# Optimization experiments

Hardware: AMD Instinct MI355X
Metric: run time of the kernel (lower is better)

The kernel has to match this reference:

```python
import jax, jax.numpy as jnp
import numpy as np

N_NODES = 50000


def _gcn_norm(edge_index, num_nodes):
    # PyG GCNConv default: add self-loops, symmetric normalization D^-1/2 A D^-1/2
    src, dst = edge_index[0], edge_index[1]
    loops = jnp.arange(num_nodes, dtype=src.dtype)
    src = jnp.concatenate([src, loops])
    dst = jnp.concatenate([dst, loops])
    deg = jax.ops.segment_sum(jnp.ones_like(src, dtype=jnp.float32), dst,
                              num_segments=num_nodes)
    dis = jnp.where(deg > 0, jax.lax.rsqrt(jnp.maximum(deg, 1.0)), 0.0)
    norm = dis[src] * dis[dst]  # [E']
    return src, dst, norm


def _gcn_conv(x, W, b, src, dst, norm, num_nodes):
    h = x @ W                                   # [N, out] transform first
    msg = h[src] * norm[:, None]                # [E', out] gather + scale
    agg = jax.ops.segment_sum(msg, dst, num_segments=num_nodes)  # scatter-add
    return agg + b


def setup_inputs() -> dict:
    key = jax.random.key(0)
    k1, k2, k3, k4 = jax.random.split(key, 4)
    n, e, d_in, d_h = N_NODES, 800000, 256, 128
    basic_block = jax.random.normal(k1, (n, d_in), dtype=jnp.float32)
    edge_index = jax.random.randint(k2, (2, e), 0, n, dtype=jnp.int64)
    W1 = jax.random.normal(k3, (d_in, d_h), dtype=jnp.float32) * (1.0 / np.sqrt(d_in))
    b1 = jnp.zeros((d_h,), dtype=jnp.float32)
    W2 = jax.random.normal(k4, (d_h, d_h), dtype=jnp.float32) * (1.0 / np.sqrt(d_h))
    b2 = jnp.zeros((d_h,), dtype=jnp.float32)
    return {"basic_block": basic_block, "edge_index": edge_index,
            "W1": W1, "b1": b1, "W2": W2, "b2": b2}


def reference(basic_block, edge_index, W1, b1, W2, b2):
    n = basic_block.shape[0]
    src, dst, norm = _gcn_norm(edge_index, n)
    x = jax.nn.relu(_gcn_conv(basic_block, W1, b1, src, dst, norm, n))
    x = _gcn_conv(x, W2, b2, src, dst, norm, n)
    return x
```

## Files before the change

kernel.cpp:

```cpp
#include <hip/hip_runtime.h>
#include <hip/hip_bf16.h>
#include <stdint.h>

#define D_H 128

typedef __bf16 bf16_t;
typedef unsigned short u16;
typedef bf16_t bf16x8 __attribute__((ext_vector_type(8)));
typedef bf16_t bf16x4 __attribute__((ext_vector_type(4)));
typedef float  f32x4  __attribute__((ext_vector_type(4)));

__global__ void k_countrank(const int* __restrict__ dst, int* __restrict__ cnt,
                            u16* __restrict__ rank, int E, int crBlocks,
                            const float* __restrict__ W1, bf16_t* __restrict__ W1h,
                            bf16_t* __restrict__ W1l, int K1,
                            const float* __restrict__ W2, bf16_t* __restrict__ W2h,
                            bf16_t* __restrict__ W2l, int K2) {
    if ((int)blockIdx.x < crBlocks) {
        int e = blockIdx.x * 256 + threadIdx.x;
        if (e < E) rank[e] = (u16)atomicAdd(&cnt[dst[e]], 1);
        return;
    }
    int id = ((int)blockIdx.x - crBlocks) * 256 + threadIdx.x;
    int n1 = K1 * 128;
    if (id < n1) {
        int k = id >> 7, n = id & 127;
        float w = W1[id];
        bf16_t h = (bf16_t)w;
        W1h[(size_t)n * K1 + k] = h;
        W1l[(size_t)n * K1 + k] = (bf16_t)(w - (float)h);
    } else if (id < n1 + K2 * 128) {
        int id2 = id - n1;
        int k = id2 >> 7, n = id2 & 127;
        float w = W2[id2];
        bf16_t h = (bf16_t)w;
        W2h[(size_t)n * K2 + k] = h;
        W2l[(size_t)n * K2 + k] = (bf16_t)(w - (float)h);
    }
}

__global__ __launch_bounds__(1024) void k_scan1(const int* __restrict__ cnt,
                                                int* __restrict__ out,
                                                int* __restrict__ bsums,
                                                float* __restrict__ dis, int N) {
    __shared__ int tmp[1024];
    int t = threadIdx.x;
    int i = blockIdx.x * 1024 + t;
    int v = (i < N) ? cnt[i] : 0;
    if (i < N) dis[i] = 1.0f / sqrtf((float)(v + 1));
    tmp[t] = v;
    __syncthreads();
    for (int d = 1; d < 1024; d <<= 1) {
        int x = (t >= d) ? tmp[t - d] : 0;
        __syncthreads();
        tmp[t] += x;
        __syncthreads();
    }
    if (i < N) out[i] = tmp[t] - v;
    if (t == 1023) bsums[blockIdx.x] = tmp[t];
}

__global__ void k_scan2(int* __restrict__ bsums, int nb) {
    __shared__ int tmp[64];
    int t = threadIdx.x;
    int v = (t < nb) ? bsums[t] : 0;
    tmp[t] = v;
    __syncthreads();
    for (int d = 1; d < 64; d <<= 1) {
        int x = (t >= d) ? tmp[t - d] : 0;
        __syncthreads();
        tmp[t] += x;
        __syncthreads();
    }
    if (t < nb) bsums[t] = tmp[t] - v;
}

__global__ __launch_bounds__(1024) void k_scan3(int* __restrict__ off,
                                                const int* __restrict__ bsums,
                                                int N, int E) {
    int i = blockIdx.x * 1024 + threadIdx.x;
    if (i < N) off[i] += bsums[blockIdx.x];
    if (i == 0) off[N] = E;
}

#define LDK 40
#define FILL_PER 2

__global__ __launch_bounds__(256) void k_mm1fill(
        const float* __restrict__ Af,
        const bf16_t* __restrict__ Wh, const bf16_t* __restrict__ Wl,
        const float* __restrict__ dis, bf16_t* __restrict__ Cb,
        int N, int K,
        const int* __restrict__ src, const int* __restrict__ dst,
        const int* __restrict__ off, const u16* __restrict__ rank,
        u16* __restrict__ csr16, int E, int totThreads) {
    __shared__ bf16_t AsH[64][LDK];
    __shared__ bf16_t AsL[64][LDK];
    __shared__ bf16_t BsH[64][LDK];
    __shared__ bf16_t BsL[64][LDK];

    const int t    = threadIdx.x;
    const int lane = t & 63;
    const int wave = t >> 6;
    const int row0 = ((int)blockIdx.x >> 1) * 64;
    const int col0 = ((int)blockIdx.x & 1) * 64;
    const int wm   = (wave & 1) * 32;
    const int wn   = (wave >> 1) * 32;
    const int fm   = lane & 15;
    const int fq   = lane >> 4;

    const int g = (int)blockIdx.x * 256 + t;
    int epos[FILL_PER];
    u16 esrc[FILL_PER];
#pragma unroll
    for (int i = 0; i < FILL_PER; i++) {
        int e = g + i * totThreads;
        if (e < E) {
            int d = dst[e];
            epos[i] = off[d] + (int)rank[e];
            esrc[i] = (u16)src[e];
        } else {
            epos[i] = -1;
            esrc[i] = 0;
        }
    }

    f32x4 acc[2][2] = {};

    for (int k0 = 0; k0 < K; k0 += 32) {
        __syncthreads();
#pragma unroll
        for (int i = 0; i < 2; i++) {
            int idx = t + i * 256;
            int r   = idx >> 3;
            int c4  = idx & 7;
            int gr  = row0 + r;
            float4 v = make_float4(0.f, 0.f, 0.f, 0.f);
            if (gr < N) v = *(const float4*)(Af + (size_t)gr * K + k0 + c4 * 4);
            bf16_t h0 = (bf16_t)v.x, h1 = (bf16_t)v.y, h2 = (bf16_t)v.z, h3 = (bf16_t)v.w;
            bf16_t l0 = (bf16_t)(v.x - (float)h0);
            bf16_t l1 = (bf16_t)(v.y - (float)h1);
            bf16_t l2 = (bf16_t)(v.z - (float)h2);
            bf16_t l3 = (bf16_t)(v.w - (float)h3);
            *(bf16x4*)&AsH[r][c4 * 4] = (bf16x4){h0, h1, h2, h3};
            *(bf16x4*)&AsL[r][c4 * 4] = (bf16x4){l0, l1, l2, l3};
        }
        {
            int r  = t >> 2;
            int c8 = t & 3;
            *(bf16x8*)&BsH[r][c8 * 8] = *(const bf16x8*)(Wh + (size_t)(col0 + r) * K + k0 + c8 * 8);
            *(bf16x8*)&BsL[r][c8 * 8] = *(const bf16x8*)(Wl + (size_t)(col0 + r) * K + k0 + c8 * 8);
        }
        __syncthreads();

        bf16x8 ah[2], al[2], bh[2], bl[2];
#pragma unroll
        for (int i = 0; i < 2; i++) {
            ah[i] = *(const bf16x8*)&AsH[wm + i * 16 + fm][fq * 8];
            al[i] = *(const bf16x8*)&AsL[wm + i * 16 + fm][fq * 8];
            bh[i] = *(const bf16x8*)&BsH[wn + i * 16 + fm][fq * 8];
            bl[i] = *(const bf16x8*)&BsL[wn + i * 16 + fm][fq * 8];
        }
#pragma unroll
        for (int mi = 0; mi < 2; mi++)
#pragma unroll
            for (int ni = 0; ni < 2; ni++) {
                acc[mi][ni] = __builtin_amdgcn_mfma_f32_16x16x32_bf16(ah[mi], bh[ni], acc[mi][ni], 0, 0, 0);
                acc[mi][ni] = __builtin_amdgcn_mfma_f32_16x16x32_bf16(ah[mi], bl[ni], acc[mi][ni], 0, 0, 0);
                acc[mi][ni] = __builtin_amdgcn_mfma_f32_16x16x32_bf16(al[mi], bh[ni], acc[mi][ni], 0, 0, 0);
            }
    }

#pragma unroll
    for (int mi = 0; mi < 2; mi++)
#pragma unroll
        for (int r = 0; r < 4; r++) {
            int grow = row0 + wm + mi * 16 + fq * 4 + r;
            if (grow < N) {
                float dr = dis[grow];
#pragma unroll
                for (int ni = 0; ni < 2; ni++)
                    Cb[(size_t)grow * D_H + col0 + wn + ni * 16 + fm] = (bf16_t)(dr * acc[mi][ni][r]);
            }
        }

#pragma unroll
    for (int i = 0; i < FILL_PER; i++)
        if (epos[i] >= 0) csr16[epos[i]] = esrc[i];
}

__global__ __launch_bounds__(256) void k_mm2(const bf16_t* __restrict__ Ah,
                                             const bf16_t* __restrict__ Al,
                                             const bf16_t* __restrict__ Wh,
                                             const bf16_t* __restrict__ Wl,
                                             const float* __restrict__ dis,
                                             bf16_t* __restrict__ Cb,
                                             int N, int K) {
    __shared__ bf16_t AsH[64][LDK];
    __shared__ bf16_t AsL[64][LDK];
    __shared__ bf16_t BsH[64][LDK];
    __shared__ bf16_t BsL[64][LDK];

    const int t    = threadIdx.x;
    const int lane = t & 63;
    const int wave = t >> 6;
    const int row0 = ((int)blockIdx.x >> 1) * 64;
    const int col0 = ((int)blockIdx.x & 1) * 64;
    const int wm   = (wave & 1) * 32;
    const int wn   = (wave >> 1) * 32;
    const int fm   = lane & 15;
    const int fq   = lane >> 4;

    f32x4 acc[2][2] = {};

    for (int k0 = 0; k0 < K; k0 += 32) {
        __syncthreads();
        {
            int r  = t >> 2;
            int c8 = t & 3;
            int gr = row0 + r;
            bf16x8 vh = {}, vl = {};
            if (gr < N) {
                vh = *(const bf16x8*)(Ah + (size_t)gr * K + k0 + c8 * 8);
                vl = *(const bf16x8*)(Al + (size_t)gr * K + k0 + c8 * 8);
            }
            *(bf16x8*)&AsH[r][c8 * 8] = vh;
            *(bf16x8*)&AsL[r][c8 * 8] = vl;
        }
        {
            int r  = t >> 2;
            int c8 = t & 3;
            *(bf16x8*)&BsH[r][c8 * 8] = *(const bf16x8*)(Wh + (size_t)(col0 + r) * K + k0 + c8 * 8);
            *(bf16x8*)&BsL[r][c8 * 8] = *(const bf16x8*)(Wl + (size_t)(col0 + r) * K + k0 + c8 * 8);
        }
        __syncthreads();

        bf16x8 ah[2], al[2], bh[2], bl[2];
#pragma unroll
        for (int i = 0; i < 2; i++) {
            ah[i] = *(const bf16x8*)&AsH[wm + i * 16 + fm][fq * 8];
            al[i] = *(const bf16x8*)&AsL[wm + i * 16 + fm][fq * 8];
            bh[i] = *(const bf16x8*)&BsH[wn + i * 16 + fm][fq * 8];
            bl[i] = *(const bf16x8*)&BsL[wn + i * 16 + fm][fq * 8];
        }
#pragma unroll
        for (int mi = 0; mi < 2; mi++)
#pragma unroll
            for (int ni = 0; ni < 2; ni++) {
                acc[mi][ni] = __builtin_amdgcn_mfma_f32_16x16x32_bf16(ah[mi], bh[ni], acc[mi][ni], 0, 0, 0);
                acc[mi][ni] = __builtin_amdgcn_mfma_f32_16x16x32_bf16(ah[mi], bl[ni], acc[mi][ni], 0, 0, 0);
                acc[mi][ni] = __builtin_amdgcn_mfma_f32_16x16x32_bf16(al[mi], bh[ni], acc[mi][ni], 0, 0, 0);
            }
    }

#pragma unroll
    for (int mi = 0; mi < 2; mi++)
#pragma unroll
        for (int r = 0; r < 4; r++) {
            int grow = row0 + wm + mi * 16 + fq * 4 + r;
            if (grow < N) {
                float dr = dis[grow];
#pragma unroll
                for (int ni = 0; ni < 2; ni++)
                    Cb[(size_t)grow * D_H + col0 + wn + ni * 16 + fm] = (bf16_t)(dr * acc[mi][ni][r]);
            }
        }
}

__global__ __launch_bounds__(256) void k_agg(const bf16_t* __restrict__ Hb,
                                             const float* __restrict__ dis,
                                             const int* __restrict__ off,
                                             const u16* __restrict__ csr16,
                                             const float4* __restrict__ bias4,
                                             float4* __restrict__ outF,
                                             bf16_t* __restrict__ outH,
                                             bf16_t* __restrict__ outL,
                                             int N, int mode) {
    const int half = threadIdx.x >> 5;
    const int lane = threadIdx.x & 31;
    const int node = blockIdx.x * 8 + half;
    if (node >= N) return;

    const size_t loff = (size_t)lane * 4;

    bf16x4 vs = *(const bf16x4*)(Hb + (size_t)node * D_H + loff);
    float4 a0 = make_float4((float)vs[0], (float)vs[1], (float)vs[2], (float)vs[3]);
    float4 a1 = {0,0,0,0}, a2 = {0,0,0,0}, a3 = {0,0,0,0};
    float4 a4 = {0,0,0,0}, a5 = {0,0,0,0}, a6 = {0,0,0,0}, a7 = {0,0,0,0};

    int p  = off[node];
    int p1 = off[node + 1];

    for (; p + 8 <= p1; p += 8) {
        int s0 = (int)csr16[p + 0], s1 = (int)csr16[p + 1];
        int s2 = (int)csr16[p + 2], s3 = (int)csr16[p + 3];
        int s4 = (int)csr16[p + 4], s5 = (int)csr16[p + 5];
        int s6 = (int)csr16[p + 6], s7 = (int)csr16[p + 7];
        bf16x4 h0 = *(const bf16x4*)(Hb + (size_t)s0 * D_H + loff);
        bf16x4 h1 = *(const bf16x4*)(Hb + (size_t)s1 * D_H + loff);
        bf16x4 h2 = *(const bf16x4*)(Hb + (size_t)s2 * D_H + loff);
        bf16x4 h3 = *(const bf16x4*)(Hb + (size_t)s3 * D_H + loff);
        bf16x4 h4 = *(const bf16x4*)(Hb + (size_t)s4 * D_H + loff);
        bf16x4 h5 = *(const bf16x4*)(Hb + (size_t)s5 * D_H + loff);
        bf16x4 h6 = *(const bf16x4*)(Hb + (size_t)s6 * D_H + loff);
        bf16x4 h7 = *(const bf16x4*)(Hb + (size_t)s7 * D_H + loff);
        a0.x += (float)h0[0]; a0.y += (float)h0[1]; a0.z += (float)h0[2]; a0.w += (float)h0[3];
        a1.x += (float)h1[0]; a1.y += (float)h1[1]; a1.z += (float)h1[2]; a1.w += (float)h1[3];
        a2.x += (float)h2[0]; a2.y += (float)h2[1]; a2.z += (float)h2[2]; a2.w += (float)h2[3];
        a3.x += (float)h3[0]; a3.y += (float)h3[1]; a3.z += (float)h3[2]; a3.w += (float)h3[3];
        a4.x += (float)h4[0]; a4.y += (float)h4[1]; a4.z += (float)h4[2]; a4.w += (float)h4[3];
        a5.x += (float)h5[0]; a5.y += (float)h5[1]; a5.z += (float)h5[2]; a5.w += (float)h5[3];
        a6.x += (float)h6[0]; a6.y += (float)h6[1]; a6.z += (float)h6[2]; a6.w += (float)h6[3];
        a7.x += (float)h7[0]; a7.y += (float)h7[1]; a7.z += (float)h7[2]; a7.w += (float)h7[3];
    }
    if (p + 4 <= p1) {
        int s0 = (int)csr16[p + 0], s1 = (int)csr16[p + 1];
        int s2 = (int)csr16[p + 2], s3 = (int)csr16[p + 3];
        bf16x4 h0 = *(const bf16x4*)(Hb + (size_t)s0 * D_H + loff);
        bf16x4 h1 = *(const bf16x4*)(Hb + (size_t)s1 * D_H + loff);
        bf16x4 h2 = *(const bf16x4*)(Hb + (size_t)s2 * D_H + loff);
        bf16x4 h3 = *(const bf16x4*)(Hb + (size_t)s3 * D_H + loff);
        a0.x += (float)h0[0]; a0.y += (float)h0[1]; a0.z += (float)h0[2]; a0.w += (float)h0[3];
        a1.x += (float)h1[0]; a1.y += (float)h1[1]; a1.z += (float)h1[2]; a1.w += (float)h1[3];
        a2.x += (float)h2[0]; a2.y += (float)h2[1]; a2.z += (float)h2[2]; a2.w += (float)h2[3];
        a3.x += (float)h3[0]; a3.y += (float)h3[1]; a3.z += (float)h3[2]; a3.w += (float)h3[3];
        p += 4;
    }
    for (; p < p1; p++) {
        int s0 = (int)csr16[p];
        bf16x4 h0 = *(const bf16x4*)(Hb + (size_t)s0 * D_H + loff);
        a0.x += (float)h0[0]; a0.y += (float)h0[1]; a0.z += (float)h0[2]; a0.w += (float)h0[3];
    }

    float4 sum;
    sum.x = ((a0.x + a1.x) + (a2.x + a3.x)) + ((a4.x + a5.x) + (a6.x + a7.x));
    sum.y = ((a0.y + a1.y) + (a2.y + a3.y)) + ((a4.y + a5.y) + (a6.y + a7.y));
    sum.z = ((a0.z + a1.z) + (a2.z + a3.z)) + ((a4.z + a5.z) + (a6.z + a7.z));
    sum.w = ((a0.w + a1.w) + (a2.w + a3.w)) + ((a4.w + a5.w) + (a6.w + a7.w));

    const float  di = dis[node];
    const float4 bv = bias4[lane];
    float vx = fmaf(di, sum.x, bv.x);
    float vy = fmaf(di, sum.y, bv.y);
    float vz = fmaf(di, sum.z, bv.z);
    float vw = fmaf(di, sum.w, bv.w);

    if (mode == 1) {
        vx = fmaxf(vx, 0.0f); vy = fmaxf(vy, 0.0f);
        vz = fmaxf(vz, 0.0f); vw = fmaxf(vw, 0.0f);
        bf16_t hx = (bf16_t)vx, hy = (bf16_t)vy, hz = (bf16_t)vz, hw = (bf16_t)vw;
        bf16_t lx = (bf16_t)(vx - (float)hx);
        bf16_t ly = (bf16_t)(vy - (float)hy);
        bf16_t lz = (bf16_t)(vz - (float)hz);
        bf16_t lw = (bf16_t)(vw - (float)hw);
        *(bf16x4*)(outH + (size_t)node * D_H + loff) = (bf16x4){hx, hy, hz, hw};
        *(bf16x4*)(outL + (size_t)node * D_H + loff) = (bf16x4){lx, ly, lz, lw};
    } else {
        outF[(size_t)node * 32 + lane] = make_float4(vx, vy, vz, vw);
    }
}

extern "C" void kernel_launch(void* const* d_in, const int* in_sizes, int n_in,
                              void* d_out, int out_size, void* d_ws, size_t ws_size,
                              hipStream_t stream) {
    const float* X  = (const float*)d_in[0];
    const int*   ei = (const int*)d_in[1];
    const float* W1 = (const float*)d_in[2];
    const float* b1 = (const float*)d_in[3];
    const float* W2 = (const float*)d_in[4];
    const float* b2 = (const float*)d_in[5];
    float* out = (float*)d_out;

    const int N  = in_sizes[0] / 256;
    const int E  = in_sizes[1] / 2;
    const int K1 = 256;

    const int* src = ei;
    const int* dst = ei + E;

    uintptr_t p = (uintptr_t)d_ws;
    auto carve = [&](size_t bytes) {
        uintptr_t q = p;
        p += (bytes + 255) & ~(size_t)255;
        return q;
    };
    int*    cnt   = (int*)carve((size_t)N * 4);
    int*    off   = (int*)carve((size_t)(N + 1) * 4);
    int*    bsums = (int*)carve(64 * 4);
    float*  dis   = (float*)carve((size_t)N * 4);
    u16*    rank  = (u16*)carve((size_t)E * 2);
    u16*    csr16 = (u16*)carve((size_t)E * 2);
    bf16_t* Hb    = (bf16_t*)carve((size_t)N * D_H * 2);
    bf16_t* X1h   = (bf16_t*)carve((size_t)N * D_H * 2);
    bf16_t* X1l   = (bf16_t*)carve((size_t)N * D_H * 2);
    bf16_t* W1h   = (bf16_t*)carve((size_t)K1 * D_H * 2);
    bf16_t* W1l   = (bf16_t*)carve((size_t)K1 * D_H * 2);
    bf16_t* W2h   = (bf16_t*)carve((size_t)D_H * D_H * 2);
    bf16_t* W2l   = (bf16_t*)carve((size_t)D_H * D_H * 2);

    const int nb = (N + 1023) / 1024;

    hipMemsetAsync(cnt, 0, (size_t)N * 4, stream);
    const int gcr   = (E + 255) / 256;
    const int gprep = (K1 * 128 + D_H * 128 + 255) / 256;
    k_countrank<<<gcr + gprep, 256, 0, stream>>>(dst, cnt, rank, E, gcr,
                                                 W1, W1h, W1l, K1,
                                                 W2, W2h, W2l, D_H);
    k_scan1<<<nb, 1024, 0, stream>>>(cnt, off, bsums, dis, N);
    k_scan2<<<1, 64, 0, stream>>>(bsums, nb);
    k_scan3<<<nb, 1024, 0, stream>>>(off, bsums, N, E);

    const int gmm = ((N + 63) / 64) * 2;
    const int gag = (N + 7) / 8;

    k_mm1fill<<<gmm, 256, 0, stream>>>(X, W1h, W1l, dis, Hb, N, K1,
                                       src, dst, off, rank, csr16, E, gmm * 256);
    k_agg<<<gag, 256, 0, stream>>>(Hb, dis, off, csr16,
                                   (const float4*)b1, nullptr, X1h, X1l, N, 1);

    k_mm2<<<gmm, 256, 0, stream>>>(X1h, X1l, W2h, W2l, dis, Hb, N, D_H);
    k_agg<<<gag, 256, 0, stream>>>(Hb, dis, off, csr16,
                                   (const float4*)b2, (float4*)out, nullptr, nullptr, N, 0);
}
```

Before: 251.4 us.

## Replace LDS-staged GEMM tiles with direct register loads and double buffering

Both GEMM kernels no longer stage A and W tiles through shared memory with two barriers per k-step. Each lane now loads its MFMA fragments straight from global memory into registers, using two register sets so the next k-tile's loads overlap the current tile's MFMAs. This removes the LDS traffic and synchronisation, but each wave reloads data that neighbouring waves also read, which puts more load on the caches. The loops hardcode K=256 and K=128 trip counts, and out-of-range rows are clamped to N-1 rather than zero-filled.

Result: slower. 295.2 us (+17.4%).

```diff
diff --git a/kernel.cpp b/kernel.cpp
--- a/kernel.cpp
+++ b/kernel.cpp
@@ -83,7 +83,6 @@
     if (i == 0) off[N] = E;
 }
 
-#define LDK 40
 #define FILL_PER 2
 
 __global__ __launch_bounds__(256) void k_mm1fill(
@@ -94,11 +93,6 @@
         const int* __restrict__ src, const int* __restrict__ dst,
         const int* __restrict__ off, const u16* __restrict__ rank,
         u16* __restrict__ csr16, int E, int totThreads) {
-    __shared__ bf16_t AsH[64][LDK];
-    __shared__ bf16_t AsL[64][LDK];
-    __shared__ bf16_t BsH[64][LDK];
-    __shared__ bf16_t BsL[64][LDK];
-
     const int t    = threadIdx.x;
     const int lane = t & 63;
     const int wave = t >> 6;
@@ -125,51 +119,67 @@
         }
     }
 
+    int ra0 = row0 + wm + fm;      if (ra0 >= N) ra0 = N - 1;
+    int ra1 = row0 + wm + 16 + fm; if (ra1 >= N) ra1 = N - 1;
+    const float*  pa0 = Af + (size_t)ra0 * K + fq * 8;
+    const float*  pa1 = Af + (size_t)ra1 * K + fq * 8;
+    const bf16_t* pb0h = Wh + (size_t)(col0 + wn + fm) * K + fq * 8;
+    const bf16_t* pb1h = Wh + (size_t)(col0 + wn + 16 + fm) * K + fq * 8;
+    const bf16_t* pb0l = Wl + (size_t)(col0 + wn + fm) * K + fq * 8;
+    const bf16_t* pb1l = Wl + (size_t)(col0 + wn + 16 + fm) * K + fq * 8;
+
     f32x4 acc[2][2] = {};
 
-    for (int k0 = 0; k0 < K; k0 += 32) {
-        __syncthreads();
-#pragma unroll
-        for (int i = 0; i < 2; i++) {
-            int idx = t + i * 256;
-            int r   = idx >> 3;
-            int c4  = idx & 7;
-            int gr  = row0 + r;
-            float4 v = make_float4(0.f, 0.f, 0.f, 0.f);
-            if (gr < N) v = *(const float4*)(Af + (size_t)gr * K + k0 + c4 * 4);
-            bf16_t h0 = (bf16_t)v.x, h1 = (bf16_t)v.y, h2 = (bf16_t)v.z, h3 = (bf16_t)v.w;
-            bf16_t l0 = (bf16_t)(v.x - (float)h0);
-            bf16_t l1 = (bf16_t)(v.y - (float)h1);
-            bf16_t l2 = (bf16_t)(v.z - (float)h2);
-            bf16_t l3 = (bf16_t)(v.w - (float)h3);
-            *(bf16x4*)&AsH[r][c4 * 4] = (bf16x4){h0, h1, h2, h3};
-            *(bf16x4*)&AsL[r][c4 * 4] = (bf16x4){l0, l1, l2, l3};
-        }
-        {
-            int r  = t >> 2;
-            int c8 = t & 3;
-            *(bf16x8*)&BsH[r][c8 * 8] = *(const bf16x8*)(Wh + (size_t)(col0 + r) * K + k0 + c8 * 8);
-            *(bf16x8*)&BsL[r][c8 * 8] = *(const bf16x8*)(Wl + (size_t)(col0 + r) * K + k0 + c8 * 8);
-        }
-        __syncthreads();
-
-        bf16x8 ah[2], al[2], bh[2], bl[2];
-#pragma unroll
-        for (int i = 0; i < 2; i++) {
-            ah[i] = *(const bf16x8*)&AsH[wm + i * 16 + fm][fq * 8];
-            al[i] = *(const bf16x8*)&AsL[wm + i * 16 + fm][fq * 8];
-            bh[i] = *(const bf16x8*)&BsH[wn + i * 16 + fm][fq * 8];
-            bl[i] = *(const bf16x8*)&BsL[wn + i * 16 + fm][fq * 8];
-        }
-#pragma unroll
-        for (int mi = 0; mi < 2; mi++)
-#pragma unroll
-            for (int ni = 0; ni < 2; ni++) {
-                acc[mi][ni] = __builtin_amdgcn_mfma_f32_16x16x32_bf16(ah[mi], bh[ni], acc[mi][ni], 0, 0, 0);
-                acc[mi][ni] = __builtin_amdgcn_mfma_f32_16x16x32_bf16(ah[mi], bl[ni], acc[mi][ni], 0, 0, 0);
-                acc[mi][ni] = __builtin_amdgcn_mfma_f32_16x16x32_bf16(al[mi], bh[ni], acc[mi][ni], 0, 0, 0);
-            }
-    }
+    float4 aA[2][2], aB[2][2];
+    bf16x8 bhA[2], blA[2], bhB[2], blB[2];
+
+#define LOAD1(kt, a, bh, bl) do {                                   \
+        int kk = (kt) * 32;                                         \
+        a[0][0] = *(const float4*)(pa0 + kk);                       \
+        a[0][1] = *(const float4*)(pa0 + kk + 4);                   \
+        a[1][0] = *(const float4*)(pa1 + kk);                       \
+        a[1][1] = *(const float4*)(pa1 + kk + 4);                   \
+        bh[0] = *(const bf16x8*)(pb0h + kk);                        \
+        bh[1] = *(const bf16x8*)(pb1h + kk);                        \
+        bl[0] = *(const bf16x8*)(pb0l + kk);                        \
+        bl[1] = *(const bf16x8*)(pb1l + kk);                        \
+    } while (0)
+
+#define COMP1(a, bh, bl) do {                                       \
+        bf16x8 ah[2], al[2];                                        \
+        _Pragma("unroll")                                           \
+        for (int mi = 0; mi < 2; mi++) {                            \
+            float v0 = a[mi][0].x, v1 = a[mi][0].y, v2 = a[mi][0].z, v3 = a[mi][0].w; \
+            float v4 = a[mi][1].x, v5 = a[mi][1].y, v6 = a[mi][1].z, v7 = a[mi][1].w; \
+            bf16_t h0=(bf16_t)v0,h1=(bf16_t)v1,h2=(bf16_t)v2,h3=(bf16_t)v3;          \
+            bf16_t h4=(bf16_t)v4,h5=(bf16_t)v5,h6=(bf16_t)v6,h7=(bf16_t)v7;          \
+            ah[mi] = (bf16x8){h0,h1,h2,h3,h4,h5,h6,h7};             \
+            al[mi] = (bf16x8){(bf16_t)(v0-(float)h0),(bf16_t)(v1-(float)h1),         \
+                              (bf16_t)(v2-(float)h2),(bf16_t)(v3-(float)h3),         \
+                              (bf16_t)(v4-(float)h4),(bf16_t)(v5-(float)h5),         \
+                              (bf16_t)(v6-(float)h6),(bf16_t)(v7-(float)h7)};        \
+        }                                                           \
+        _Pragma("unroll")                                           \
+        for (int mi = 0; mi < 2; mi++)                              \
+            _Pragma("unroll")                                       \
+            for (int ni = 0; ni < 2; ni++) {                        \
+                acc[mi][ni] = __builtin_amdgcn_mfma_f32_16x16x32_bf16(ah[mi], bh[ni], acc[mi][ni], 0, 0, 0); \
+                acc[mi][ni] = __builtin_amdgcn_mfma_f32_16x16x32_bf16(ah[mi], bl[ni], acc[mi][ni], 0, 0, 0); \
+                acc[mi][ni] = __builtin_amdgcn_mfma_f32_16x16x32_bf16(al[mi], bh[ni], acc[mi][ni], 0, 0, 0); \
+            }                                                       \
+    } while (0)
+
+    const int KT = K >> 5;
+    LOAD1(0, aA, bhA, blA);
+#pragma unroll
+    for (int kt = 0; kt < 8; kt += 2) {
+        LOAD1(kt + 1, aB, bhB, blB);
+        COMP1(aA, bhA, blA);
+        if (kt + 2 < KT) LOAD1(kt + 2, aA, bhA, blA);
+        COMP1(aB, bhB, blB);
+    }
+#undef LOAD1
+#undef COMP1
 
 #pragma unroll
     for (int mi = 0; mi < 2; mi++)
@@ -196,11 +206,6 @@
                                              const float* __restrict__ dis,
                                              bf16_t* __restrict__ Cb,
                                              int N, int K) {
-    __shared__ bf16_t AsH[64][LDK];
-    __shared__ bf16_t AsL[64][LDK];
-    __shared__ bf16_t BsH[64][LDK];
-    __shared__ bf16_t BsL[64][LDK];
-
     const int t    = threadIdx.x;
     const int lane = t & 63;
     const int wave = t >> 6;
@@ -211,47 +216,56 @@
     const int fm   = lane & 15;
     const int fq   = lane >> 4;
 
+    int ra0 = row0 + wm + fm;      if (ra0 >= N) ra0 = N - 1;
+    int ra1 = row0 + wm + 16 + fm; if (ra1 >= N) ra1 = N - 1;
+    const bf16_t* pa0h = Ah + (size_t)ra0 * K + fq * 8;
+    const bf16_t* pa1h = Ah + (size_t)ra1 * K + fq * 8;
+    const bf16_t* pa0l = Al + (size_t)ra0 * K + fq * 8;
+    const bf16_t* pa1l = Al + (size_t)ra1 * K + fq * 8;
+    const bf16_t* pb0h = Wh + (size_t)(col0 + wn + fm) * K + fq * 8;
+    const bf16_t* pb1h = Wh + (size_t)(col0 + wn + 16 + fm) * K + fq * 8;
+    const bf16_t* pb0l = Wl + (size_t)(col0 + wn + fm) * K + fq * 8;
+    const bf16_t* pb1l = Wl + (size_t)(col0 + wn + 16 + fm) * K + fq * 8;
+
     f32x4 acc[2][2] = {};
 
-    for (int k0 = 0; k0 < K; k0 += 32) {
-        __syncthreads();
-        {
-            int r  = t >> 2;
-            int c8 = t & 3;
-            int gr = row0 + r;
-            bf16x8 vh = {}, vl = {};
-            if (gr < N) {
-                vh = *(const bf16x8*)(Ah + (size_t)gr * K + k0 + c8 * 8);
-                vl = *(const bf16x8*)(Al + (size_t)gr * K + k0 + c8 * 8);
-            }
-            *(bf16x8*)&AsH[r][c8 * 8] = vh;
-            *(bf16x8*)&AsL[r][c8 * 8] = vl;
-        }
-        {
-            int r  = t >> 2;
-            int c8 = t & 3;
-            *(bf16x8*)&BsH[r][c8 * 8] = *(const bf16x8*)(Wh + (size_t)(col0 + r) * K + k0 + c8 * 8);
-            *(bf16x8*)&BsL[r][c8 * 8] = *(const bf16x8*)(Wl + (size_t)(col0 + r) * K + k0 + c8 * 8);
-        }
-        __syncthreads();
-
-        bf16x8 ah[2], al[2], bh[2], bl[2];
-#pragma unroll
-        for (int i = 0; i < 2; i++) {
-            ah[i] = *(const bf16x8*)&AsH[wm + i * 16 + fm][fq * 8];
-            al[i] = *(const bf16x8*)&AsL[wm + i * 16 + fm][fq * 8];
-            bh[i] = *(const bf16x8*)&BsH[wn + i * 16 + fm][fq * 8];
-            bl[i] = *(const bf16x8*)&BsL[wn + i * 16 + fm][fq * 8];
-        }
-#pragma unroll
-        for (int mi = 0; mi < 2; mi++)
-#pragma unroll
-            for (int ni = 0; ni < 2; ni++) {
-                acc[mi][ni] = __builtin_amdgcn_mfma_f32_16x16x32_bf16(ah[mi], bh[ni], acc[mi][ni], 0, 0, 0);
-                acc[mi][ni] = __builtin_amdgcn_mfma_f32_16x16x32_bf16(ah[mi], bl[ni], acc[mi][ni], 0, 0, 0);
-                acc[mi][ni] = __builtin_amdgcn_mfma_f32_16x16x32_bf16(al[mi], bh[ni], acc[mi][ni], 0, 0, 0);
-            }
-    }
+    bf16x8 ahA[2], alA[2], bhA[2], blA[2];
+    bf16x8 ahB[2], alB[2], bhB[2], blB[2];
+
+#define LOAD2(kt, ah, al, bh, bl) do {                              \
+        int kk = (kt) * 32;                                         \
+        ah[0] = *(const bf16x8*)(pa0h + kk);                        \
+        ah[1] = *(const bf16x8*)(pa1h + kk);                        \
+        al[0] = *(const bf16x8*)(pa0l + kk);                        \
+        al[1] = *(const bf16x8*)(pa1l + kk);                        \
+        bh[0] = *(const bf16x8*)(pb0h + kk);                        \
+        bh[1] = *(const bf16x8*)(pb1h + kk);                        \
+        bl[0] = *(const bf16x8*)(pb0l + kk);                        \
+        bl[1] = *(const bf16x8*)(pb1l + kk);                        \
+    } while (0)
+
+#define COMP2(ah, al, bh, bl) do {                                  \
+        _Pragma("unroll")                                           \
+        for (int mi = 0; mi < 2; mi++)                              \
+            _Pragma("unroll")                                       \
+            for (int ni = 0; ni < 2; ni++) {                        \
+                acc[mi][ni] = __builtin_amdgcn_mfma_f32_16x16x32_bf16(ah[mi], bh[ni], acc[mi][ni], 0, 0, 0); \
+                acc[mi][ni] = __builtin_amdgcn_mfma_f32_16x16x32_bf16(ah[mi], bl[ni], acc[mi][ni], 0, 0, 0); \
+                acc[mi][ni] = __builtin_amdgcn_mfma_f32_16x16x32_bf16(al[mi], bh[ni], acc[mi][ni], 0, 0, 0); \
+            }                                                       \
+    } while (0)
+
+    const int KT = K >> 5;
+    LOAD2(0, ahA, alA, bhA, blA);
+#pragma unroll
+    for (int kt = 0; kt < 4; kt += 2) {
+        LOAD2(kt + 1, ahB, alB, bhB, blB);
+        COMP2(ahA, alA, bhA, blA);
+        if (kt + 2 < KT) LOAD2(kt + 2, ahA, alA, bhA, blA);
+        COMP2(ahB, alB, bhB, blB);
+    }
+#undef LOAD2
+#undef COMP2
 
 #pragma unroll
     for (int mi = 0; mi < 2; mi++)
```

## Split aggregation feature dimension into four chunks across separate blocks

Applied to the files above, without the earlier changes.

The aggregation kernel now assigns 8 threads per node covering a 32-feature chunk, and the grid is replicated four times, once per feature chunk, with chunk-major block ordering. All concurrently running blocks then gather the same 64-byte slice of each source row, so the active gather working set is a quarter of the feature matrix and is meant to stay resident in cache. The cost is that each node's CSR offsets and indices are read four times, and each gather is a narrow 64-byte segment instead of a full 256-byte row.

Result: slower. 271.3 us (+7.9%).

```diff
diff --git a/kernel.cpp b/kernel.cpp
--- a/kernel.cpp
+++ b/kernel.cpp
@@ -275,15 +275,18 @@
                                              float4* __restrict__ outF,
                                              bf16_t* __restrict__ outH,
                                              bf16_t* __restrict__ outL,
-                                             int N, int mode) {
-    const int half = threadIdx.x >> 5;
-    const int lane = threadIdx.x & 31;
-    const int node = blockIdx.x * 8 + half;
+                                             int N, int mode, int nbase) {
+    const int chunk = (int)blockIdx.x / nbase;
+    const int nblk  = (int)blockIdx.x % nbase;
+    const int slot  = threadIdx.x >> 3;
+    const int lane8 = threadIdx.x & 7;
+    const int node  = nblk * 32 + slot;
     if (node >= N) return;
 
-    const size_t loff = (size_t)lane * 4;
-
-    bf16x4 vs = *(const bf16x4*)(Hb + (size_t)node * D_H + loff);
+    const int  fidx = chunk * 32 + lane8 * 4;
+    const bf16_t* Hc = Hb + fidx;
+
+    bf16x4 vs = *(const bf16x4*)(Hc + (size_t)node * D_H);
     float4 a0 = make_float4((float)vs[0], (float)vs[1], (float)vs[2], (float)vs[3]);
     float4 a1 = {0,0,0,0}, a2 = {0,0,0,0}, a3 = {0,0,0,0};
     float4 a4 = {0,0,0,0}, a5 = {0,0,0,0}, a6 = {0,0,0,0}, a7 = {0,0,0,0};
@@ -296,14 +299,14 @@
         int s2 = (int)csr16[p + 2], s3 = (int)csr16[p + 3];
         int s4 = (int)csr16[p + 4], s5 = (int)csr16[p + 5];
         int s6 = (int)csr16[p + 6], s7 = (int)csr16[p + 7];
-        bf16x4 h0 = *(const bf16x4*)(Hb + (size_t)s0 * D_H + loff);
-        bf16x4 h1 = *(const bf16x4*)(Hb + (size_t)s1 * D_H + loff);
-        bf16x4 h2 = *(const bf16x4*)(Hb + (size_t)s2 * D_H + loff);
-        bf16x4 h3 = *(const bf16x4*)(Hb + (size_t)s3 * D_H + loff);
-        bf16x4 h4 = *(const bf16x4*)(Hb + (size_t)s4 * D_H + loff);
-        bf16x4 h5 = *(const bf16x4*)(Hb + (size_t)s5 * D_H + loff);
-        bf16x4 h6 = *(const bf16x4*)(Hb + (size_t)s6 * D_H + loff);
-        bf16x4 h7 = *(const bf16x4*)(Hb + (size_t)s7 * D_H + loff);
+        bf16x4 h0 = *(const bf16x4*)(Hc + (size_t)s0 * D_H);
+        bf16x4 h1 = *(const bf16x4*)(Hc + (size_t)s1 * D_H);
+        bf16x4 h2 = *(const bf16x4*)(Hc + (size_t)s2 * D_H);
+        bf16x4 h3 = *(const bf16x4*)(Hc + (size_t)s3 * D_H);
+        bf16x4 h4 = *(const bf16x4*)(Hc + (size_t)s4 * D_H);
+        bf16x4 h5 = *(const bf16x4*)(Hc + (size_t)s5 * D_H);
+        bf16x4 h6 = *(const bf16x4*)(Hc + (size_t)s6 * D_H);
+        bf16x4 h7 = *(const bf16x4*)(Hc + (size_t)s7 * D_H);
         a0.x += (float)h0[0]; a0.y += (float)h0[1]; a0.z += (float)h0[2]; a0.w += (float)h0[3];
         a1.x += (float)h1[0]; a1.y += (float)h1[1]; a1.z += (float)h1[2]; a1.w += (float)h1[3];
         a2.x += (float)h2[0]; a2.y += (float)h2[1]; a2.z += (float)h2[2]; a2.w += (float)h2[3];
@@ -316,10 +319,10 @@
     if (p + 4 <= p1) {
         int s0 = (int)csr16[p + 0], s1 = (int)csr16[p + 1];
         int s2 = (int)csr16[p + 2], s3 = (int)csr16[p + 3];
-        bf16x4 h0 = *(const bf16x4*)(Hb + (size_t)s0 * D_H + loff);
-        bf16x4 h1 = *(const bf16x4*)(Hb + (size_t)s1 * D_H + loff);
-        bf16x4 h2 = *(const bf16x4*)(Hb + (size_t)s2 * D_H + loff);
-        bf16x4 h3 = *(const bf16x4*)(Hb + (size_t)s3 * D_H + loff);
+        bf16x4 h0 = *(const bf16x4*)(Hc + (size_t)s0 * D_H);
+        bf16x4 h1 = *(const bf16x4*)(Hc + (size_t)s1 * D_H);
+        bf16x4 h2 = *(const bf16x4*)(Hc + (size_t)s2 * D_H);
+        bf16x4 h3 = *(const bf16x4*)(Hc + (size_t)s3 * D_H);
         a0.x += (float)h0[0]; a0.y += (float)h0[1]; a0.z += (float)h0[2]; a0.w += (float)h0[3];
         a1.x += (float)h1[0]; a1.y += (float)h1[1]; a1.z += (float)h1[2]; a1.w += (float)h1[3];
         a2.x += (float)h2[0]; a2.y += (float)h2[1]; a2.z += (float)h2[2]; a2.w += (float)h2[3];
@@ -328,7 +331,7 @@
     }
     for (; p < p1; p++) {
         int s0 = (int)csr16[p];
-        bf16x4 h0 = *(const bf16x4*)(Hb + (size_t)s0 * D_H + loff);
+        bf16x4 h0 = *(const bf16x4*)(Hc + (size_t)s0 * D_H);
         a0.x += (float)h0[0]; a0.y += (float)h0[1]; a0.z += (float)h0[2]; a0.w += (float)h0[3];
     }
 
@@ -339,7 +342,7 @@
     sum.w = ((a0.w + a1.w) + (a2.w + a3.w)) + ((a4.w + a5.w) + (a6.w + a7.w));
 
     const float  di = dis[node];
-    const float4 bv = bias4[lane];
+    const float4 bv = bias4[chunk * 8 + lane8];
     float vx = fmaf(di, sum.x, bv.x);
     float vy = fmaf(di, sum.y, bv.y);
     float vz = fmaf(di, sum.z, bv.z);
@@ -353,10 +356,10 @@
         bf16_t ly = (bf16_t)(vy - (float)hy);
         bf16_t lz = (bf16_t)(vz - (float)hz);
         bf16_t lw = (bf16_t)(vw - (float)hw);
-        *(bf16x4*)(outH + (size_t)node * D_H + loff) = (bf16x4){hx, hy, hz, hw};
-        *(bf16x4*)(outL + (size_t)node * D_H + loff) = (bf16x4){lx, ly, lz, lw};
+        *(bf16x4*)(outH + (size_t)node * D_H + fidx) = (bf16x4){hx, hy, hz, hw};
+        *(bf16x4*)(outL + (size_t)node * D_H + fidx) = (bf16x4){lx, ly, lz, lw};
     } else {
-        outF[(size_t)node * 32 + lane] = make_float4(vx, vy, vz, vw);
+        outF[(size_t)node * 32 + chunk * 8 + lane8] = make_float4(vx, vy, vz, vw);
     }
 }
 
@@ -410,15 +413,16 @@
     k_scan2<<<1, 64, 0, stream>>>(bsums, nb);
     k_scan3<<<nb, 1024, 0, stream>>>(off, bsums, N, E);
 
-    const int gmm = ((N + 63) / 64) * 2;
-    const int gag = (N + 7) / 8;
+    const int gmm   = ((N + 63) / 64) * 2;
+    const int nbase = (N + 31) / 32;
+    const int gag   = nbase * 4;
 
     k_mm1fill<<<gmm, 256, 0, stream>>>(X, W1h, W1l, dis, Hb, N, K1,
                                        src, dst, off, rank, csr16, E, gmm * 256);
     k_agg<<<gag, 256, 0, stream>>>(Hb, dis, off, csr16,
-                                   (const float4*)b1, nullptr, X1h, X1l, N, 1);
+                                   (const float4*)b1, nullptr, X1h, X1l, N, 1, nbase);
 
     k_mm2<<<gmm, 256, 0, stream>>>(X1h, X1l, W2h, W2l, dis, Hb, N, D_H);
     k_agg<<<gag, 256, 0, stream>>>(Hb, dis, off, csr16,
-                                   (const float4*)b2, (float4*)out, nullptr, nullptr, N, 0);
-}
+                                   (const float4*)b2, (float4*)out, nullptr, nullptr, N, 0, nbase);
+}
```

## Register-prefetch next GEMM k-tile and widen aggregation to 16 lanes per node

Applied to the files above, without the earlier changes.

Both GEMM kernels now load the next k-tile from global memory into registers while the current tile is computed, so global load latency overlaps with the MFMA work. Separately, the aggregation kernel assigns 16 lanes per node with 16-byte bf16x8 gathers instead of 32 lanes with 8-byte loads, doubling nodes per block and halving gather instruction count. The trade-off is more live registers and less unrolling depth per node (4 instead of 8 edges in flight).

After: 269.5 us. +7.2%, slower.

```diff
diff --git a/kernel.cpp b/kernel.cpp
--- a/kernel.cpp
+++ b/kernel.cpp
@@ -125,32 +125,46 @@
         }
     }
 
+    const int ar0 = t >> 3;
+    const int ar1 = (t >> 3) + 32;
+    const int ac4 = t & 7;
+    const int br  = t >> 2;
+    const int bc8 = t & 3;
+    const int gr0 = row0 + ar0;
+    const int gr1 = row0 + ar1;
+
+    float4 rA0, rA1;
+    bf16x8 rBh, rBl;
+    const float4 fz = make_float4(0.f, 0.f, 0.f, 0.f);
+
+    auto gload = [&](int k0) {
+        rA0 = (gr0 < N) ? *(const float4*)(Af + (size_t)gr0 * K + k0 + ac4 * 4) : fz;
+        rA1 = (gr1 < N) ? *(const float4*)(Af + (size_t)gr1 * K + k0 + ac4 * 4) : fz;
+        rBh = *(const bf16x8*)(Wh + (size_t)(col0 + br) * K + k0 + bc8 * 8);
+        rBl = *(const bf16x8*)(Wl + (size_t)(col0 + br) * K + k0 + bc8 * 8);
+    };
+    auto lstore = [&]() {
+        float4 v = rA0;
+        bf16_t h0 = (bf16_t)v.x, h1 = (bf16_t)v.y, h2 = (bf16_t)v.z, h3 = (bf16_t)v.w;
+        *(bf16x4*)&AsH[ar0][ac4 * 4] = (bf16x4){h0, h1, h2, h3};
+        *(bf16x4*)&AsL[ar0][ac4 * 4] = (bf16x4){(bf16_t)(v.x - (float)h0), (bf16_t)(v.y - (float)h1),
+                                                (bf16_t)(v.z - (float)h2), (bf16_t)(v.w - (float)h3)};
+        v = rA1;
+        h0 = (bf16_t)v.x; h1 = (bf16_t)v.y; h2 = (bf16_t)v.z; h3 = (bf16_t)v.w;
+        *(bf16x4*)&AsH[ar1][ac4 * 4] = (bf16x4){h0, h1, h2, h3};
+        *(bf16x4*)&AsL[ar1][ac4 * 4] = (bf16x4){(bf16_t)(v.x - (float)h0), (bf16_t)(v.y - (float)h1),
+                                                (bf16_t)(v.z - (float)h2), (bf16_t)(v.w - (float)h3)};
+        *(bf16x8*)&BsH[br][bc8 * 8] = rBh;
+        *(bf16x8*)&BsL[br][bc8 * 8] = rBl;
+    };
+
     f32x4 acc[2][2] = {};
 
+    gload(0);
     for (int k0 = 0; k0 < K; k0 += 32) {
         __syncthreads();
-#pragma unroll
-        for (int i = 0; i < 2; i++) {
-            int idx = t + i * 256;
-            int r   = idx >> 3;
-            int c4  = idx & 7;
-            int gr  = row0 + r;
-            float4 v = make_float4(0.f, 0.f, 0.f, 0.f);
-            if (gr < N) v = *(const float4*)(Af + (size_t)gr * K + k0 + c4 * 4);
-            bf16_t h0 = (bf16_t)v.x, h1 = (bf16_t)v.y, h2 = (bf16_t)v.z, h3 = (bf16_t)v.w;
-            bf16_t l0 = (bf16_t)(v.x - (float)h0);
-            bf16_t l1 = (bf16_t)(v.y - (float)h1);
-            bf16_t l2 = (bf16_t)(v.z - (float)h2);
-            bf16_t l3 = (bf16_t)(v.w - (float)h3);
-            *(bf16x4*)&AsH[r][c4 * 4] = (bf16x4){h0, h1, h2, h3};
-            *(bf16x4*)&AsL[r][c4 * 4] = (bf16x4){l0, l1, l2, l3};
-        }
-        {
-            int r  = t >> 2;
-            int c8 = t & 3;
-            *(bf16x8*)&BsH[r][c8 * 8] = *(const bf16x8*)(Wh + (size_t)(col0 + r) * K + k0 + c8 * 8);
-            *(bf16x8*)&BsL[r][c8 * 8] = *(const bf16x8*)(Wl + (size_t)(col0 + r) * K + k0 + c8 * 8);
-        }
+        lstore();
+        if (k0 + 32 < K) gload(k0 + 32);
         __syncthreads();
 
         bf16x8 ah[2], al[2], bh[2], bl[2];
@@ -211,28 +225,32 @@
     const int fm   = lane & 15;
     const int fq   = lane >> 4;
 
+    const int r8  = t >> 2;
+    const int c8  = t & 3;
+    const int gr  = row0 + r8;
+
+    bf16x8 rAh, rAl, rBh, rBl;
+    auto gload = [&](int k0) {
+        bf16x8 z = {};
+        rAh = (gr < N) ? *(const bf16x8*)(Ah + (size_t)gr * K + k0 + c8 * 8) : z;
+        rAl = (gr < N) ? *(const bf16x8*)(Al + (size_t)gr * K + k0 + c8 * 8) : z;
+        rBh = *(const bf16x8*)(Wh + (size_t)(col0 + r8) * K + k0 + c8 * 8);
+        rBl = *(const bf16x8*)(Wl + (size_t)(col0 + r8) * K + k0 + c8 * 8);
+    };
+    auto lstore = [&]() {
+        *(bf16x8*)&AsH[r8][c8 * 8] = rAh;
+        *(bf16x8*)&AsL[r8][c8 * 8] = rAl;
+        *(bf16x8*)&BsH[r8][c8 * 8] = rBh;
+        *(bf16x8*)&BsL[r8][c8 * 8] = rBl;
+    };
+
     f32x4 acc[2][2] = {};
 
+    gload(0);
     for (int k0 = 0; k0 < K; k0 += 32) {
         __syncthreads();
-        {
-            int r  = t >> 2;
-            int c8 = t & 3;
-            int gr = row0 + r;
-            bf16x8 vh = {}, vl = {};
-            if (gr < N) {
-                vh = *(const bf16x8*)(Ah + (size_t)gr * K + k0 + c8 * 8);
-                vl = *(const bf16x8*)(Al + (size_t)gr * K + k0 + c8 * 8);
-            }
-            *(bf16x8*)&AsH[r][c8 * 8] = vh;
-            *(bf16x8*)&AsL[r][c8 * 8] = vl;
-        }
-        {
-            int r  = t >> 2;
-            int c8 = t & 3;
-            *(bf16x8*)&BsH[r][c8 * 8] = *(const bf16x8*)(Wh + (size_t)(col0 + r) * K + k0 + c8 * 8);
-            *(bf16x8*)&BsL[r][c8 * 8] = *(const bf16x8*)(Wl + (size_t)(col0 + r) * K + k0 + c8 * 8);
-        }
+        lstore();
+        if (k0 + 32 < K) gload(k0 + 32);
         __syncthreads();
 
         bf16x8 ah[2], al[2], bh[2], bl[2];
@@ -276,87 +294,80 @@
                                              bf16_t* __restrict__ outH,
                                              bf16_t* __restrict__ outL,
                                              int N, int mode) {
-    const int half = threadIdx.x >> 5;
-    const int lane = threadIdx.x & 31;
-    const int node = blockIdx.x * 8 + half;
+    const int slot = threadIdx.x >> 4;
+    const int lane = threadIdx.x & 15;
+    const int node = blockIdx.x * 16 + slot;
     if (node >= N) return;
 
-    const size_t loff = (size_t)lane * 4;
-
-    bf16x4 vs = *(const bf16x4*)(Hb + (size_t)node * D_H + loff);
-    float4 a0 = make_float4((float)vs[0], (float)vs[1], (float)vs[2], (float)vs[3]);
-    float4 a1 = {0,0,0,0}, a2 = {0,0,0,0}, a3 = {0,0,0,0};
-    float4 a4 = {0,0,0,0}, a5 = {0,0,0,0}, a6 = {0,0,0,0}, a7 = {0,0,0,0};
+    const bf16_t* Hrow = Hb + (size_t)lane * 8;
+
+    float a0[8], a1[8], a2[8], a3[8];
+    {
+        bf16x8 v = *(const bf16x8*)(Hrow + (size_t)node * D_H);
+#pragma unroll
+        for (int j = 0; j < 8; j++) { a0[j] = (float)v[j]; a1[j] = 0.f; a2[j] = 0.f; a3[j] = 0.f; }
+    }
 
     int p  = off[node];
     int p1 = off[node + 1];
 
-    for (; p + 8 <= p1; p += 8) {
+    for (; p + 4 <= p1; p += 4) {
         int s0 = (int)csr16[p + 0], s1 = (int)csr16[p + 1];
         int s2 = (int)csr16[p + 2], s3 = (int)csr16[p + 3];
-        int s4 = (int)csr16[p + 4], s5 = (int)csr16[p + 5];
-        int s6 = (int)csr16[p + 6], s7 = (int)csr16[p + 7];
-        bf16x4 h0 = *(const bf16x4*)(Hb + (size_t)s0 * D_H + loff);
-        bf16x4 h1 = *(const bf16x4*)(Hb + (size_t)s1 * D_H + loff);
-        bf16x4 h2 = *(const bf16x4*)(Hb + (size_t)s2 * D_H + loff);
-        bf16x4 h3 = *(const bf16x4*)(Hb + (size_t)s3 * D_H + loff);
-        bf16x4 h4 = *(const bf16x4*)(Hb + (size_t)s4 * D_H + loff);
-        bf16x4 h5 = *(const bf16x4*)(Hb + (size_t)s5 * D_H + loff);
-        bf16x4 h6 = *(const bf16x4*)(Hb + (size_t)s6 * D_H + loff);
-        bf16x4 h7 = *(const bf16x4*)(Hb + (size_t)s7 * D_H + loff);
-        a0.x += (float)h0[0]; a0.y += (float)h0[1]; a0.z += (float)h0[2]; a0.w += (float)h0[3];
-        a1.x += (float)h1[0]; a1.y += (float)h1[1]; a1.z += (float)h1[2]; a1.w += (float)h1[3];
-        a2.x += (float)h2[0]; a2.y += (float)h2[1]; a2.z += (float)h2[2]; a2.w += (float)h2[3];
-        a3.x += (float)h3[0]; a3.y += (float)h3[1]; a3.z += (float)h3[2]; a3.w += (float)h3[3];
-        a4.x += (float)h4[0]; a4.y += (float)h4[1]; a4.z += (float)h4[2]; a4.w += (float)h4[3];
-        a5.x += (float)h5[0]; a5.y += (float)h5[1]; a5.z += (float)h5[2]; a5.w += (float)h5[3];
-        a6.x += (float)h6[0]; a6.y += (float)h6[1]; a6.z += (float)h6[2]; a6.w += (float)h6[3];
-        a7.x += (float)h7[0]; a7.y += (float)h7[1]; a7.z += (float)h7[2]; a7.w += (float)h7[3];
-    }
-    if (p + 4 <= p1) {
+        bf16x8 h0 = *(const bf16x8*)(Hrow + (size_t)s0 * D_H);
+        bf16x8 h1 = *(const bf16x8*)(Hrow + (size_t)s1 * D_H);
+        bf16x8 h2 = *(const bf16x8*)(Hrow + (size_t)s2 * D_H);
+        bf16x8 h3 = *(const bf16x8*)(Hrow + (size_t)s3 * D_H);
+#pragma unroll
+        for (int j = 0; j < 8; j++) {
+            a0[j] += (float)h0[j];
+            a1[j] += (float)h1[j];
+            a2[j] += (float)h2[j];
+            a3[j] += (float)h3[j];
+        }
+    }
+    if (p + 2 <= p1) {
         int s0 = (int)csr16[p + 0], s1 = (int)csr16[p + 1];
-        int s2 = (int)csr16[p + 2], s3 = (int)csr16[p + 3];
-        bf16x4 h0 = *(const bf16x4*)(Hb + (size_t)s0 * D_H + loff);
-        bf16x4 h1 = *(const bf16x4*)(Hb + (size_t)s1 * D_H + loff);
-        bf16x4 h2 = *(const bf16x4*)(Hb + (size_t)s2 * D_H + loff);
-        bf16x4 h3 = *(const bf16x4*)(Hb + (size_t)s3 * D_H + loff);
-        a0.x += (float)h0[0]; a0.y += (float)h0[1]; a0.z += (float)h0[2]; a0.w += (float)h0[3];
-        a1.x += (float)h1[0]; a1.y += (float)h1[1]; a1.z += (float)h1[2]; a1.w += (float)h1[3];
-        a2.x += (float)h2[0]; a2.y += (float)h2[1]; a2.z += (float)h2[2]; a2.w += (float)h2[3];
-        a3.x += (float)h3[0]; a3.y += (float)h3[1]; a3.z += (float)h3[2]; a3.w += (float)h3[3];
-        p += 4;
-    }
-    for (; p < p1; p++) {
+        bf16x8 h0 = *(const bf16x8*)(Hrow + (size_t)s0 * D_H);
+        bf16x8 h1 = *(const bf16x8*)(Hrow + (size_t)s1 * D_H);
+#pragma unroll
+        for (int j = 0; j < 8; j++) { a0[j] += (float)h0[j]; a1[j] += (float)h1[j]; }
+        p += 2;
+    }
+    if (p < p1) {
         int s0 = (int)csr16[p];
-        bf16x4 h0 = *(const bf16x4*)(Hb + (size_t)s0 * D_H + loff);
-        a0.x += (float)h0[0]; a0.y += (float)h0[1]; a0.z += (float)h0[2]; a0.w += (float)h0[3];
-    }
-
-    float4 sum;
-    sum.x = ((a0.x + a1.x) + (a2.x + a3.x)) + ((a4.x + a5.x) + (a6.x + a7.x));
-    sum.y = ((a0.y + a1.y) + (a2.y + a3.y)) + ((a4.y + a5.y) + (a6.y + a7.y));
-    sum.z = ((a0.z + a1.z) + (a2.z + a3.z)) + ((a4.z + a5.z) + (a6.z + a7.z));
-    sum.w = ((a0.w + a1.w) + (a2.w + a3.w)) + ((a4.w + a5.w) + (a6.w + a7.w));
+        bf16x8 h0 = *(const bf16x8*)(Hrow + (size_t)s0 * D_H);
+#pragma unroll
+        for (int j = 0; j < 8; j++) a2[j] += (float)h0[j];
+    }
+
+    float sum[8];
+#pragma unroll
+    for (int j = 0; j < 8; j++) sum[j] = (a0[j] + a1[j]) + (a2[j] + a3[j]);
 
     const float  di = dis[node];
-    const float4 bv = bias4[lane];
-    float vx = fmaf(di, sum.x, bv.x);
-    float vy = fmaf(di, sum.y, bv.y);
-    float vz = fmaf(di, sum.z, bv.z);
-    float vw = fmaf(di, sum.w, bv.w);
+    const float4 b0 = bias4[lane * 2];
+    const float4 b1 = bias4[lane * 2 + 1];
+    float v0 = fmaf(di, sum[0], b0.x), v1 = fmaf(di, sum[1], b0.y);
+    float v2 = fmaf(di, sum[2], b0.z), v3 = fmaf(di, sum[3], b0.w);
+    float v4 = fmaf(di, sum[4], b1.x), v5 = fmaf(di, sum[5], b1.y);
+    float v6 = fmaf(di, sum[6], b1.z), v7 = fmaf(di, sum[7], b1.w);
 
     if (mode == 1) {
-        vx = fmaxf(vx, 0.0f); vy = fmaxf(vy, 0.0f);
-        vz = fmaxf(vz, 0.0f); vw = fmaxf(vw, 0.0f);
-        bf16_t hx = (bf16_t)vx, hy = (bf16_t)vy, hz = (bf16_t)vz, hw = (bf16_t)vw;
-        bf16_t lx = (bf16_t)(vx - (float)hx);
-        bf16_t ly = (bf16_t)(vy - (float)hy);
-        bf16_t lz = (bf16_t)(vz - (float)hz);
-        bf16_t lw = (bf16_t)(vw - (float)hw);
-        *(bf16x4*)(outH + (size_t)node * D_H + loff) = (bf16x4){hx, hy, hz, hw};
-        *(bf16x4*)(outL + (size_t)node * D_H + loff) = (bf16x4){lx, ly, lz, lw};
+        v0 = fmaxf(v0, 0.f); v1 = fmaxf(v1, 0.f); v2 = fmaxf(v2, 0.f); v3 = fmaxf(v3, 0.f);
+        v4 = fmaxf(v4, 0.f); v5 = fmaxf(v5, 0.f); v6 = fmaxf(v6, 0.f); v7 = fmaxf(v7, 0.f);
+        bf16_t h0 = (bf16_t)v0, h1 = (bf16_t)v1, h2 = (bf16_t)v2, h3 = (bf16_t)v3;
+        bf16_t h4 = (bf16_t)v4, h5 = (bf16_t)v5, h6 = (bf16_t)v6, h7 = (bf16_t)v7;
+        *(bf16x8*)(outH + (size_t)node * D_H + lane * 8) =
+            (bf16x8){h0, h1, h2, h3, h4, h5, h6, h7};
+        *(bf16x8*)(outL + (size_t)node * D_H + lane * 8) =
+            (bf16x8){(bf16_t)(v0 - (float)h0), (bf16_t)(v1 - (float)h1),
+                     (bf16_t)(v2 - (float)h2), (bf16_t)(v3 - (float)h3),
+                     (bf16_t)(v4 - (float)h4), (bf16_t)(v5 - (float)h5),
+                     (bf16_t)(v6 - (float)h6), (bf16_t)(v7 - (float)h7)};
     } else {
-        outF[(size_t)node * 32 + lane] = make_float4(vx, vy, vz, vw);
+        outF[(size_t)node * 32 + lane * 2]     = make_float4(v0, v1, v2, v3);
+        outF[(size_t)node * 32 + lane * 2 + 1] = make_float4(v4, v5, v6, v7);
     }
 }
 
@@ -411,7 +422,7 @@
     k_scan3<<<nb, 1024, 0, stream>>>(off, bsums, N, E);
 
     const int gmm = ((N + 63) / 64) * 2;
-    const int gag = (N + 7) / 8;
+    const int gag = (N + 15) / 16;
 
     k_mm1fill<<<gmm, 256, 0, stream>>>(X, W1h, W1l, dis, Hb, N, K1,
                                        src, dst, off, rank, csr16, E, gmm * 256);
```
